# Kernel tuning notes

Measured on AMD Instinct MI355X. Metric: run time of the kernel, lower is better.

Reference implementation:

```python
import jax, jax.numpy as jnp
import numpy as np

SPARSE_COMPRESSION_RATIO = 0.5  # config.sparse_compression_ratio


def setup_inputs() -> dict:
    key = jax.random.key(0)
    kv_cache = jax.random.normal(key, (2, 32, 4096, 128), dtype=jnp.float32)
    return {"kv_cache": kv_cache}


def reference(kv_cache):
    # elements_to_keep = int(numel * (1 - ratio))
    total = kv_cache.size
    k = int(total * (1.0 - SPARSE_COMPRESSION_RATIO))
    flat = kv_cache.reshape(-1)
    # torch.topk(|x|, k, largest=True) -> indices of k largest magnitudes
    _, top_idx = jax.lax.top_k(jnp.abs(flat), k)
    # scatter mask, then elementwise multiply (zeros out non-top-k entries)
    mask = jnp.zeros((total,), dtype=jnp.bool_).at[top_idx].set(True)
    return kv_cache * mask.reshape(kv_cache.shape)
```

## Files before the change

kernel.cpp:

```cpp
#include <hip/hip_runtime.h>
#include <stdint.h>


#define NTHR 256
#define MASK31 0x7fffffffu

#define SH_OFF    0
#define SH_BINS   8192
#define CH_OFF    8192
#define CH_BINS   4096
#define SCL_OFF   12288
#define L3_OFF    12320
#define L3_CAP    4096
#define PAIRS_OFF (L3_OFF + 2 * L3_CAP)
#define PAIRS_CAP 4194304
#define ZERO_WORDS (SCL_OFF + 32)

#define GC_CAP    4096
#define TIE_CAP   1024

__global__ void zero_ws_kernel(uint32_t* __restrict__ ws) {
    int i = blockIdx.x * blockDim.x + threadIdx.x;
    if (i < ZERO_WORDS) ws[i] = 0;
}

__global__ void sample_hist_kernel(const uint4* __restrict__ xv, long long n4,
                                   uint32_t* __restrict__ ws) {
    __shared__ uint32_t lh[SH_BINS];
    for (int i = threadIdx.x; i < SH_BINS; i += NTHR) lh[i] = 0;
    __syncthreads();
    long long S4 = n4 >> 5;
    long long T = (long long)gridDim.x * NTHR;
    for (long long s = (long long)blockIdx.x * NTHR + threadIdx.x; s < S4; s += T) {
        uint4 v = xv[s << 5];
        atomicAdd(&lh[(v.x & MASK31) >> 18], 1u);
        atomicAdd(&lh[(v.y & MASK31) >> 18], 1u);
        atomicAdd(&lh[(v.z & MASK31) >> 18], 1u);
        atomicAdd(&lh[(v.w & MASK31) >> 18], 1u);
    }
    __syncthreads();
    for (int i = threadIdx.x; i < SH_BINS; i += NTHR)
        if (lh[i]) atomicAdd(&ws[SH_OFF + i], lh[i]);
}

__global__ void sel_bracket_kernel(uint32_t* __restrict__ ws,
                                   uint32_t ksmM, uint32_t kspM) {
    __shared__ uint32_t lh[SH_BINS];
    __shared__ uint32_t csum[NTHR];
    __shared__ uint32_t cpre[NTHR];
    __shared__ int sBHi, sB1;
    for (int i = threadIdx.x; i < SH_BINS; i += NTHR) lh[i] = ws[SH_OFF + i];
    if (threadIdx.x == 0) { sBHi = -1; sB1 = -1; }
    __syncthreads();
    uint32_t s = 0;
    for (int i = 0; i < 32; ++i) s += lh[threadIdx.x * 32 + i];
    csum[threadIdx.x] = s;
    __syncthreads();
    if (threadIdx.x == 0) {
        uint32_t run = 0;
        for (int c = NTHR - 1; c >= 0; --c) { cpre[c] = run; run += csum[c]; }
    }
    __syncthreads();
    {
        int c = threadIdx.x;
        int hitHi = -1, hitB1 = -1;
        uint32_t excl = cpre[c];
        for (int bb = c * 32 + 31; bb >= c * 32; --bb) {
            uint32_t cnt = lh[bb];
            uint32_t incl = excl + cnt;
            if (hitHi < 0 && incl >= ksmM) hitHi = bb;
            if (hitB1 < 0 && excl >= kspM) hitB1 = bb;
            excl = incl;
        }
        if (hitHi >= 0) atomicMax(&sBHi, hitHi);
        if (hitB1 >= 0) atomicMax(&sB1, hitB1);
    }
    __syncthreads();
    if (threadIdx.x == 0) {
        int bHi = sBHi < 0 ? 0 : sBHi;
        int bLo = sB1 + 1;
        if (bLo > bHi) bLo = bHi;
        if (bLo < 0) bLo = 0;
        int span = bHi - bLo + 1;
        int clog = 0; while ((1 << clog) < span) ++clog;
        int spanBits = 18 + clog;
        int shift1 = spanBits > 12 ? spanBits - 12 : 0;
        ws[SCL_OFF + 0] = (uint32_t)bLo;
        ws[SCL_OFF + 1] = (uint32_t)bHi;
        ws[SCL_OFF + 2] = (uint32_t)shift1;
        ws[SCL_OFF + 3] = ((uint32_t)bLo) << 18;
    }
}

__global__ void fused_main_kernel(const uint32_t* __restrict__ x,
                                  uint32_t* __restrict__ out, long long n,
                                  uint32_t* __restrict__ ws) {
    __shared__ uint2 stage[GC_CAP];
    __shared__ uint32_t cnt, sHi, base;
    uint32_t bLo = ws[SCL_OFF + 0], bHi = ws[SCL_OFF + 1];
    if (threadIdx.x == 0) { cnt = 0; sHi = 0; }
    __syncthreads();
    uint32_t myHi = 0;
    long long n4 = n >> 2;
    const uint4* xv = (const uint4*)x;
    uint4* ov = (uint4*)out;
    long long stride = (long long)gridDim.x * NTHR;
    for (long long i = (long long)blockIdx.x * NTHR + threadIdx.x; i < n4; i += stride) {
        uint4 v = xv[i];
        uint32_t base4 = (uint32_t)(i << 2);
        uint4 o;
        uint32_t u, b;
        u = v.x & MASK31; b = u >> 18;
        if (b > bHi) { o.x = v.x; ++myHi; }
        else { o.x = 0u; if (b >= bLo) { uint32_t p = atomicAdd(&cnt, 1u); if (p < GC_CAP) stage[p] = make_uint2(v.x, base4 + 0); } }
        u = v.y & MASK31; b = u >> 18;
        if (b > bHi) { o.y = v.y; ++myHi; }
        else { o.y = 0u; if (b >= bLo) { uint32_t p = atomicAdd(&cnt, 1u); if (p < GC_CAP) stage[p] = make_uint2(v.y, base4 + 1); } }
        u = v.z & MASK31; b = u >> 18;
        if (b > bHi) { o.z = v.z; ++myHi; }
        else { o.z = 0u; if (b >= bLo) { uint32_t p = atomicAdd(&cnt, 1u); if (p < GC_CAP) stage[p] = make_uint2(v.z, base4 + 2); } }
        u = v.w & MASK31; b = u >> 18;
        if (b > bHi) { o.w = v.w; ++myHi; }
        else { o.w = 0u; if (b >= bLo) { uint32_t p = atomicAdd(&cnt, 1u); if (p < GC_CAP) stage[p] = make_uint2(v.w, base4 + 3); } }
        ov[i] = o;
    }
    if (blockIdx.x == 0 && threadIdx.x < (int)(n & 3)) {
        long long idx = (n4 << 2) + threadIdx.x;
        uint32_t v = x[idx];
        uint32_t u = v & MASK31, b = u >> 18;
        uint32_t o = 0u;
        if (b > bHi) { o = v; ++myHi; }
        else if (b >= bLo) { uint32_t p = atomicAdd(&cnt, 1u); if (p < GC_CAP) stage[p] = make_uint2(v, (uint32_t)idx); }
        out[idx] = o;
    }
    if (myHi) atomicAdd(&sHi, myHi);
    __syncthreads();
    if (threadIdx.x == 0) {
        uint32_t c = cnt < GC_CAP ? cnt : GC_CAP;
        cnt = c;
        base = atomicAdd(&ws[SCL_OFF + 5], c);
        if (sHi) atomicAdd(&ws[SCL_OFF + 4], sHi);
    }
    __syncthreads();
    uint2* pairs = (uint2*)(ws + PAIRS_OFF);
    uint32_t c = cnt, b0 = base;
    for (uint32_t q = threadIdx.x; q < c; q += NTHR)
        if (b0 + q < PAIRS_CAP) pairs[b0 + q] = stage[q];
}

__global__ void cand_hist_kernel(uint32_t* __restrict__ ws) {
    __shared__ uint32_t lh[CH_BINS];
    uint32_t G = ws[SCL_OFF + 5]; if (G > PAIRS_CAP) G = PAIRS_CAP;
    uint32_t spanBase = ws[SCL_OFF + 3], shift1 = ws[SCL_OFF + 2];
    for (int i = threadIdx.x; i < CH_BINS; i += NTHR) lh[i] = 0;
    __syncthreads();
    const uint2* pairs = (const uint2*)(ws + PAIRS_OFF);
    uint32_t stride = gridDim.x * NTHR;
    for (uint32_t i = blockIdx.x * NTHR + threadIdx.x; i < G; i += stride) {
        uint32_t u = pairs[i].x & MASK31;
        atomicAdd(&lh[((u - spanBase) >> shift1) & (CH_BINS - 1)], 1u);
    }
    __syncthreads();
    for (int i = threadIdx.x; i < CH_BINS; i += NTHR)
        if (lh[i]) atomicAdd(&ws[CH_OFF + i], lh[i]);
}

__global__ void sel_gather_kernel(uint32_t* __restrict__ ws, uint32_t k) {
    __shared__ uint32_t lh[CH_BINS];
    __shared__ uint32_t csum[NTHR];
    __shared__ uint32_t cpre[NTHR];
    __shared__ uint32_t sBase2, sRem2;
    for (int i = threadIdx.x; i < CH_BINS; i += NTHR) lh[i] = ws[CH_OFF + i];
    __syncthreads();
    uint32_t kp = k - ws[SCL_OFF + 4];
    uint32_t s = 0;
    for (int i = 0; i < 16; ++i) s += lh[threadIdx.x * 16 + i];
    csum[threadIdx.x] = s;
    __syncthreads();
    if (threadIdx.x == 0) {
        uint32_t run = 0;
        for (int c = NTHR - 1; c >= 0; --c) { cpre[c] = run; run += csum[c]; }
    }
    __syncthreads();
    if (cpre[threadIdx.x] < kp && kp <= cpre[threadIdx.x] + csum[threadIdx.x]) {
        uint32_t excl = cpre[threadIdx.x];
        for (int bb = threadIdx.x * 16 + 15; bb >= threadIdx.x * 16; --bb) {
            uint32_t cnt = lh[bb];
            if (excl + cnt >= kp) {
                sBase2 = ws[SCL_OFF + 3] + (((uint32_t)bb) << ws[SCL_OFF + 2]);
                sRem2 = kp - excl;
                break;
            }
            excl += cnt;
        }
    }
    __syncthreads();
    if (threadIdx.x == 0) { ws[SCL_OFF + 6] = sBase2; ws[SCL_OFF + 7] = sRem2; }
    uint32_t base2 = sBase2;
    uint32_t width = 1u << ws[SCL_OFF + 2];
    uint32_t G = ws[SCL_OFF + 5]; if (G > PAIRS_CAP) G = PAIRS_CAP;
    const uint2* pairs = (const uint2*)(ws + PAIRS_OFF);
    uint2* l3 = (uint2*)(ws + L3_OFF);
    uint32_t stride = gridDim.x * NTHR;
    for (uint32_t i = blockIdx.x * NTHR + threadIdx.x; i < G; i += stride) {
        uint2 pr = pairs[i];
        uint32_t u = pr.x & MASK31;
        if (u - base2 < width) {
            uint32_t p = atomicAdd(&ws[SCL_OFF + 8], 1u);
            if (p < L3_CAP) l3[p] = pr;
        }
    }
}

__global__ void final_fixup_kernel(uint32_t* __restrict__ ws,
                                   uint32_t* __restrict__ out) {
    __shared__ uint32_t lh[CH_BINS];
    __shared__ uint32_t csum[NTHR];
    __shared__ uint32_t cpre[NTHR];
    __shared__ uint32_t tieIdx[TIE_CAP];
    __shared__ uint32_t tieCnt, sT, sJ, sTieMax;
    uint32_t c3 = ws[SCL_OFF + 8]; if (c3 > L3_CAP) c3 = L3_CAP;
    uint32_t base2 = ws[SCL_OFF + 6], rem2 = ws[SCL_OFF + 7];
    for (int i = threadIdx.x; i < CH_BINS; i += NTHR) lh[i] = 0;
    if (threadIdx.x == 0) tieCnt = 0;
    __syncthreads();
    const uint2* l3 = (const uint2*)(ws + L3_OFF);
    for (uint32_t i = threadIdx.x; i < c3; i += NTHR) {
        uint32_t u = l3[i].x & MASK31;
        atomicAdd(&lh[(u - base2) & (CH_BINS - 1)], 1u);
    }
    __syncthreads();
    uint32_t s = 0;
    for (int i = 0; i < 16; ++i) s += lh[threadIdx.x * 16 + i];
    csum[threadIdx.x] = s;
    __syncthreads();
    if (threadIdx.x == 0) {
        uint32_t run = 0;
        for (int c = NTHR - 1; c >= 0; --c) { cpre[c] = run; run += csum[c]; }
    }
    __syncthreads();
    if (cpre[threadIdx.x] < rem2 && rem2 <= cpre[threadIdx.x] + csum[threadIdx.x]) {
        uint32_t excl = cpre[threadIdx.x];
        for (int bb = threadIdx.x * 16 + 15; bb >= threadIdx.x * 16; --bb) {
            uint32_t cnt = lh[bb];
            if (excl + cnt >= rem2) { sT = base2 + (uint32_t)bb; sJ = rem2 - excl; break; }
            excl += cnt;
        }
    }
    __syncthreads();
    uint32_t t = sT;
    for (uint32_t i = threadIdx.x; i < c3; i += NTHR) {
        uint2 pr = l3[i];
        if ((pr.x & MASK31) == t) {
            uint32_t p = atomicAdd(&tieCnt, 1u);
            if (p < TIE_CAP) tieIdx[p] = pr.y;
        }
    }
    __syncthreads();
    if (threadIdx.x == 0) {
        uint32_t m = tieCnt < TIE_CAP ? tieCnt : TIE_CAP;
        for (uint32_t a = 1; a < m; ++a) {
            uint32_t v = tieIdx[a]; int bp = (int)a - 1;
            while (bp >= 0 && tieIdx[bp] > v) { tieIdx[bp + 1] = tieIdx[bp]; --bp; }
            tieIdx[bp + 1] = v;
        }
        uint32_t j = sJ;
        if (j > m) j = m;
        sJ = j;
        sTieMax = (j > 0) ? tieIdx[j - 1] : 0u;
    }
    __syncthreads();
    uint32_t j = sJ, tieMax = sTieMax;
    uint32_t G = ws[SCL_OFF + 5]; if (G > PAIRS_CAP) G = PAIRS_CAP;
    const uint2* pairs = (const uint2*)(ws + PAIRS_OFF);
    uint32_t stride = gridDim.x * NTHR;
    for (uint32_t i = blockIdx.x * NTHR + threadIdx.x; i < G; i += stride) {
        uint2 pr = pairs[i];
        uint32_t u = pr.x & MASK31;
        bool keep = (u > t) || (u == t && j > 0 && pr.y <= tieMax);
        if (keep) out[pr.y] = pr.x;
    }
}

extern "C" void kernel_launch(void* const* d_in, const int* in_sizes, int n_in,
                              void* d_out, int out_size, void* d_ws, size_t ws_size,
                              hipStream_t stream) {
    const uint32_t* x = (const uint32_t*)d_in[0];
    uint32_t* out = (uint32_t*)d_out;
    uint32_t* ws = (uint32_t*)d_ws;
    long long n = (long long)in_sizes[0];

    const double ratio = 0.5;
    long long k = (long long)((double)n * (1.0 - ratio));
    if (k < 1) k = 1;
    if (k > n) k = n;

    long long n4 = n >> 2;
    long long S = (n4 >> 5) << 2;
    long long ks = (long long)((double)k * ((double)S / (double)n));
    const long long M = 4500;
    uint32_t ksmM = (uint32_t)((ks - M) < 1 ? 1 : (ks - M));
    uint32_t kspM = (uint32_t)((ks + M) > S ? S : (ks + M));

    zero_ws_kernel<<<(ZERO_WORDS + NTHR - 1) / NTHR, NTHR, 0, stream>>>(ws);
    sample_hist_kernel<<<512, NTHR, 0, stream>>>((const uint4*)x, n4, ws);
    sel_bracket_kernel<<<1, NTHR, 0, stream>>>(ws, ksmM, kspM);
    fused_main_kernel<<<2048, NTHR, 0, stream>>>(x, out, n, ws);
    cand_hist_kernel<<<256, NTHR, 0, stream>>>(ws);
    sel_gather_kernel<<<256, NTHR, 0, stream>>>(ws, (uint32_t)k);
    final_fixup_kernel<<<256, NTHR, 0, stream>>>(ws, out);
}
```

Measured before the change: 154.7 us.

## Restructure main pass into one-chunk-per-block with global overflow for candidates

The main filter kernel now gives each block exactly one chunk of four uint4 loads per thread, issued together, in place of a grid-stride loop over 2048 blocks. The shared staging buffer shrinks from 4096 to 512 pairs, and overflow spills straight to the global pair list through an atomic, so more blocks fit per CU. The sample histogram now staggers its sampled offsets within each 32-vector stride, and several small kernels get smaller grids. The aim is more memory-level parallelism and occupancy, at the cost of possible global atomic contention when a block has many candidates.

```diff
diff --git a/kernel.cpp b/kernel.cpp
--- a/kernel.cpp
+++ b/kernel.cpp
@@ -16,7 +16,7 @@
 #define PAIRS_CAP 4194304
 #define ZERO_WORDS (SCL_OFF + 32)
 
-#define GC_CAP    4096
+#define GC_CAP    512
 #define TIE_CAP   1024
 
 __global__ void zero_ws_kernel(uint32_t* __restrict__ ws) {
@@ -32,7 +32,8 @@
     long long S4 = n4 >> 5;
     long long T = (long long)gridDim.x * NTHR;
     for (long long s = (long long)blockIdx.x * NTHR + threadIdx.x; s < S4; s += T) {
-        uint4 v = xv[s << 5];
+        long long idx4 = (s << 5) | (s & 31);
+        uint4 v = xv[idx4];
         atomicAdd(&lh[(v.x & MASK31) >> 18], 1u);
         atomicAdd(&lh[(v.y & MASK31) >> 18], 1u);
         atomicAdd(&lh[(v.z & MASK31) >> 18], 1u);
@@ -92,60 +93,80 @@
     }
 }
 
-__global__ void fused_main_kernel(const uint32_t* __restrict__ x,
-                                  uint32_t* __restrict__ out, long long n,
-                                  uint32_t* __restrict__ ws) {
+__global__ __launch_bounds__(NTHR, 6)
+void fused_main_kernel(const uint32_t* __restrict__ x, uint32_t* __restrict__ out,
+                       long long n, uint32_t* __restrict__ ws) {
     __shared__ uint2 stage[GC_CAP];
-    __shared__ uint32_t cnt, sHi, base;
-    uint32_t bLo = ws[SCL_OFF + 0], bHi = ws[SCL_OFF + 1];
-    if (threadIdx.x == 0) { cnt = 0; sHi = 0; }
+    __shared__ uint32_t cnt, sHi, sBase;
+    const uint32_t bLo = ws[SCL_OFF + 0], bHi = ws[SCL_OFF + 1];
+    const uint32_t bSpan = bHi - bLo;
+    if (threadIdx.x == 0) { cnt = 0u; sHi = 0u; }
     __syncthreads();
     uint32_t myHi = 0;
+    uint2* __restrict__ gpairs = (uint2*)(ws + PAIRS_OFF);
+
+    const uint4* __restrict__ xv = (const uint4*)x;
+    uint4* __restrict__ ov = (uint4*)out;
     long long n4 = n >> 2;
-    const uint4* xv = (const uint4*)x;
-    uint4* ov = (uint4*)out;
-    long long stride = (long long)gridDim.x * NTHR;
-    for (long long i = (long long)blockIdx.x * NTHR + threadIdx.x; i < n4; i += stride) {
-        uint4 v = xv[i];
-        uint32_t base4 = (uint32_t)(i << 2);
-        uint4 o;
-        uint32_t u, b;
-        u = v.x & MASK31; b = u >> 18;
-        if (b > bHi) { o.x = v.x; ++myHi; }
-        else { o.x = 0u; if (b >= bLo) { uint32_t p = atomicAdd(&cnt, 1u); if (p < GC_CAP) stage[p] = make_uint2(v.x, base4 + 0); } }
-        u = v.y & MASK31; b = u >> 18;
-        if (b > bHi) { o.y = v.y; ++myHi; }
-        else { o.y = 0u; if (b >= bLo) { uint32_t p = atomicAdd(&cnt, 1u); if (p < GC_CAP) stage[p] = make_uint2(v.y, base4 + 1); } }
-        u = v.z & MASK31; b = u >> 18;
-        if (b > bHi) { o.z = v.z; ++myHi; }
-        else { o.z = 0u; if (b >= bLo) { uint32_t p = atomicAdd(&cnt, 1u); if (p < GC_CAP) stage[p] = make_uint2(v.z, base4 + 2); } }
-        u = v.w & MASK31; b = u >> 18;
-        if (b > bHi) { o.w = v.w; ++myHi; }
-        else { o.w = 0u; if (b >= bLo) { uint32_t p = atomicAdd(&cnt, 1u); if (p < GC_CAP) stage[p] = make_uint2(v.w, base4 + 3); } }
-        ov[i] = o;
-    }
-    if (blockIdx.x == 0 && threadIdx.x < (int)(n & 3)) {
-        long long idx = (n4 << 2) + threadIdx.x;
-        uint32_t v = x[idx];
-        uint32_t u = v & MASK31, b = u >> 18;
-        uint32_t o = 0u;
-        if (b > bHi) { o = v; ++myHi; }
-        else if (b >= bLo) { uint32_t p = atomicAdd(&cnt, 1u); if (p < GC_CAP) stage[p] = make_uint2(v, (uint32_t)idx); }
-        out[idx] = o;
-    }
+    long long nChunks = n4 / (NTHR * 4);
+
+#define PUSH_PAIR(val, eidx) { \
+    uint32_t p_ = atomicAdd(&cnt, 1u); \
+    uint2 pr_ = make_uint2((val), (eidx)); \
+    if (p_ < GC_CAP) stage[p_] = pr_; \
+    else { uint32_t g_ = atomicAdd(&ws[SCL_OFF + 5], 1u); if (g_ < PAIRS_CAP) gpairs[g_] = pr_; } }
+
+#define COMP(val, eidx) { \
+    uint32_t u_ = (val) & MASK31; uint32_t b_ = u_ >> 18; \
+    uint32_t hi_ = (b_ > bHi) ? 1u : 0u; myHi += hi_; \
+    if (b_ - bLo <= bSpan) PUSH_PAIR((val), (eidx)); \
+    (val) = hi_ ? (val) : 0u; }
+
+    if ((long long)blockIdx.x < nChunks) {
+        long long i0 = (long long)blockIdx.x * (NTHR * 4) + threadIdx.x;
+        uint4 v0 = xv[i0];
+        uint4 v1 = xv[i0 + NTHR];
+        uint4 v2 = xv[i0 + 2 * NTHR];
+        uint4 v3 = xv[i0 + 3 * NTHR];
+        uint32_t e0 = (uint32_t)(i0 << 2);
+        uint32_t e1 = e0 + NTHR * 4;
+        uint32_t e2 = e0 + 2 * NTHR * 4;
+        uint32_t e3 = e0 + 3 * NTHR * 4;
+        COMP(v0.x, e0 + 0) COMP(v0.y, e0 + 1) COMP(v0.z, e0 + 2) COMP(v0.w, e0 + 3)
+        COMP(v1.x, e1 + 0) COMP(v1.y, e1 + 1) COMP(v1.z, e1 + 2) COMP(v1.w, e1 + 3)
+        COMP(v2.x, e2 + 0) COMP(v2.y, e2 + 1) COMP(v2.z, e2 + 2) COMP(v2.w, e2 + 3)
+        COMP(v3.x, e3 + 0) COMP(v3.y, e3 + 1) COMP(v3.z, e3 + 2) COMP(v3.w, e3 + 3)
+        ov[i0]            = v0;
+        ov[i0 + NTHR]     = v1;
+        ov[i0 + 2 * NTHR] = v2;
+        ov[i0 + 3 * NTHR] = v3;
+    }
+
+    long long tailStart = nChunks * (NTHR * 4) * 4;
+    if (blockIdx.x == 0) {
+        for (long long idx = tailStart + threadIdx.x; idx < n; idx += NTHR) {
+            uint32_t v = x[idx];
+            uint32_t u_ = v & MASK31, b_ = u_ >> 18;
+            uint32_t hi_ = (b_ > bHi) ? 1u : 0u; myHi += hi_;
+            if (b_ - bLo <= bSpan) PUSH_PAIR(v, (uint32_t)idx);
+            out[idx] = hi_ ? v : 0u;
+        }
+    }
+
     if (myHi) atomicAdd(&sHi, myHi);
     __syncthreads();
     if (threadIdx.x == 0) {
         uint32_t c = cnt < GC_CAP ? cnt : GC_CAP;
         cnt = c;
-        base = atomicAdd(&ws[SCL_OFF + 5], c);
+        sBase = atomicAdd(&ws[SCL_OFF + 5], c);
         if (sHi) atomicAdd(&ws[SCL_OFF + 4], sHi);
     }
     __syncthreads();
-    uint2* pairs = (uint2*)(ws + PAIRS_OFF);
-    uint32_t c = cnt, b0 = base;
+    uint32_t c = cnt, b0 = sBase;
     for (uint32_t q = threadIdx.x; q < c; q += NTHR)
-        if (b0 + q < PAIRS_CAP) pairs[b0 + q] = stage[q];
+        if (b0 + q < PAIRS_CAP) gpairs[b0 + q] = stage[q];
+#undef COMP
+#undef PUSH_PAIR
 }
 
 __global__ void cand_hist_kernel(uint32_t* __restrict__ ws) {
@@ -302,11 +323,14 @@
     uint32_t ksmM = (uint32_t)((ks - M) < 1 ? 1 : (ks - M));
     uint32_t kspM = (uint32_t)((ks + M) > S ? S : (ks + M));
 
+    long long nChunks = n4 / (NTHR * 4);
+    int grid = (int)(nChunks < 1 ? 1 : nChunks);
+
     zero_ws_kernel<<<(ZERO_WORDS + NTHR - 1) / NTHR, NTHR, 0, stream>>>(ws);
-    sample_hist_kernel<<<512, NTHR, 0, stream>>>((const uint4*)x, n4, ws);
+    sample_hist_kernel<<<128, NTHR, 0, stream>>>((const uint4*)x, n4, ws);
     sel_bracket_kernel<<<1, NTHR, 0, stream>>>(ws, ksmM, kspM);
-    fused_main_kernel<<<2048, NTHR, 0, stream>>>(x, out, n, ws);
-    cand_hist_kernel<<<256, NTHR, 0, stream>>>(ws);
-    sel_gather_kernel<<<256, NTHR, 0, stream>>>(ws, (uint32_t)k);
-    final_fixup_kernel<<<256, NTHR, 0, stream>>>(ws, out);
-}
+    fused_main_kernel<<<grid, NTHR, 0, stream>>>(x, out, n, ws);
+    cand_hist_kernel<<<128, NTHR, 0, stream>>>(ws);
+    sel_gather_kernel<<<128, NTHR, 0, stream>>>(ws, (uint32_t)k);
+    final_fixup_kernel<<<128, NTHR, 0, stream>>>(ws, out);
+}
```

New measurement: 264.6 us. +71.1%, slower.

## Replace candidate compaction with two-pass histogram refine and rank-based tie fixup

Applied to the files above, without the earlier changes.

The single pass that wrote the output and staged every bracket candidate into a global pairs buffer is replaced by two streaming passes over the input. The first pass builds a 1024-bin histogram of the bracketed magnitude range and counts elements above it. A one-block select kernel then picks a narrow threshold bin, and the second pass writes the output while collecting only that bin's few elements. A single-block kernel resolves the boundary bin with an O(m²) rank by value and index. The sample histogram also switches to a strided, spread-out sampling layout. This removes the large candidate shuffling and the multi-kernel gather at the cost of reading the input twice.

```diff
diff --git a/kernel.cpp b/kernel.cpp
--- a/kernel.cpp
+++ b/kernel.cpp
@@ -7,17 +7,12 @@
 
 #define SH_OFF    0
 #define SH_BINS   8192
-#define CH_OFF    8192
-#define CH_BINS   4096
-#define SCL_OFF   12288
-#define L3_OFF    12320
-#define L3_CAP    4096
-#define PAIRS_OFF (L3_OFF + 2 * L3_CAP)
-#define PAIRS_CAP 4194304
-#define ZERO_WORDS (SCL_OFF + 32)
-
-#define GC_CAP    4096
-#define TIE_CAP   1024
+#define BH_OFF    8192
+#define BH_BINS   1024
+#define SCL_OFF   9216
+#define PAIRS_OFF 9232
+#define PAIRS_CAP 8192
+#define ZERO_WORDS (SCL_OFF + 16)
 
 __global__ void zero_ws_kernel(uint32_t* __restrict__ ws) {
     int i = blockIdx.x * blockDim.x + threadIdx.x;
@@ -32,7 +27,9 @@
     long long S4 = n4 >> 5;
     long long T = (long long)gridDim.x * NTHR;
     for (long long s = (long long)blockIdx.x * NTHR + threadIdx.x; s < S4; s += T) {
-        uint4 v = xv[s << 5];
+        long long g = s >> 6;
+        long long idx4 = g * 2048 + ((g & 31) << 6) + (s & 63);
+        uint4 v = xv[idx4];
         atomicAdd(&lh[(v.x & MASK31) >> 18], 1u);
         atomicAdd(&lh[(v.y & MASK31) >> 18], 1u);
         atomicAdd(&lh[(v.z & MASK31) >> 18], 1u);
@@ -81,204 +78,146 @@
         int bLo = sB1 + 1;
         if (bLo > bHi) bLo = bHi;
         if (bLo < 0) bLo = 0;
-        int span = bHi - bLo + 1;
-        int clog = 0; while ((1 << clog) < span) ++clog;
+        int sbins = bHi - bLo + 1;
+        int clog = 0; while ((1 << clog) < sbins) ++clog;
         int spanBits = 18 + clog;
-        int shift1 = spanBits > 12 ? spanBits - 12 : 0;
-        ws[SCL_OFF + 0] = (uint32_t)bLo;
-        ws[SCL_OFF + 1] = (uint32_t)bHi;
+        int shift1 = spanBits - 10;
+        if (shift1 < 0) shift1 = 0;
+        ws[SCL_OFF + 0] = ((uint32_t)bLo) << 18;
+        ws[SCL_OFF + 1] = ((uint32_t)(bHi + 1)) << 18;
         ws[SCL_OFF + 2] = (uint32_t)shift1;
-        ws[SCL_OFF + 3] = ((uint32_t)bLo) << 18;
-    }
-}
-
-__global__ void fused_main_kernel(const uint32_t* __restrict__ x,
-                                  uint32_t* __restrict__ out, long long n,
+    }
+}
+
+__global__ void pass1_hist_kernel(const uint32_t* __restrict__ x, long long n,
                                   uint32_t* __restrict__ ws) {
-    __shared__ uint2 stage[GC_CAP];
-    __shared__ uint32_t cnt, sHi, base;
-    uint32_t bLo = ws[SCL_OFF + 0], bHi = ws[SCL_OFF + 1];
-    if (threadIdx.x == 0) { cnt = 0; sHi = 0; }
-    __syncthreads();
+    __shared__ uint32_t lh[BH_BINS];
+    for (int i = threadIdx.x; i < BH_BINS; i += NTHR) lh[i] = 0;
+    __syncthreads();
+    const uint32_t uLo = ws[SCL_OFF + 0];
+    const uint32_t uHi = ws[SCL_OFF + 1];
+    const uint32_t shift1 = ws[SCL_OFF + 2];
+    const uint32_t span = uHi - uLo;
     uint32_t myHi = 0;
+
+#define DOH(comp) { uint32_t u_ = (comp) & MASK31; \
+    myHi += (u_ >= uHi) ? 1u : 0u; \
+    uint32_t d_ = u_ - uLo; \
+    if (d_ < span) atomicAdd(&lh[(d_ >> shift1) & (BH_BINS - 1)], 1u); }
+
     long long n4 = n >> 2;
-    const uint4* xv = (const uint4*)x;
-    uint4* ov = (uint4*)out;
+    const uint4* __restrict__ xv = (const uint4*)x;
     long long stride = (long long)gridDim.x * NTHR;
     for (long long i = (long long)blockIdx.x * NTHR + threadIdx.x; i < n4; i += stride) {
         uint4 v = xv[i];
-        uint32_t base4 = (uint32_t)(i << 2);
-        uint4 o;
-        uint32_t u, b;
-        u = v.x & MASK31; b = u >> 18;
-        if (b > bHi) { o.x = v.x; ++myHi; }
-        else { o.x = 0u; if (b >= bLo) { uint32_t p = atomicAdd(&cnt, 1u); if (p < GC_CAP) stage[p] = make_uint2(v.x, base4 + 0); } }
-        u = v.y & MASK31; b = u >> 18;
-        if (b > bHi) { o.y = v.y; ++myHi; }
-        else { o.y = 0u; if (b >= bLo) { uint32_t p = atomicAdd(&cnt, 1u); if (p < GC_CAP) stage[p] = make_uint2(v.y, base4 + 1); } }
-        u = v.z & MASK31; b = u >> 18;
-        if (b > bHi) { o.z = v.z; ++myHi; }
-        else { o.z = 0u; if (b >= bLo) { uint32_t p = atomicAdd(&cnt, 1u); if (p < GC_CAP) stage[p] = make_uint2(v.z, base4 + 2); } }
-        u = v.w & MASK31; b = u >> 18;
-        if (b > bHi) { o.w = v.w; ++myHi; }
-        else { o.w = 0u; if (b >= bLo) { uint32_t p = atomicAdd(&cnt, 1u); if (p < GC_CAP) stage[p] = make_uint2(v.w, base4 + 3); } }
-        ov[i] = o;
-    }
-    if (blockIdx.x == 0 && threadIdx.x < (int)(n & 3)) {
-        long long idx = (n4 << 2) + threadIdx.x;
-        uint32_t v = x[idx];
-        uint32_t u = v & MASK31, b = u >> 18;
-        uint32_t o = 0u;
-        if (b > bHi) { o = v; ++myHi; }
-        else if (b >= bLo) { uint32_t p = atomicAdd(&cnt, 1u); if (p < GC_CAP) stage[p] = make_uint2(v, (uint32_t)idx); }
-        out[idx] = o;
-    }
-    if (myHi) atomicAdd(&sHi, myHi);
-    __syncthreads();
-    if (threadIdx.x == 0) {
-        uint32_t c = cnt < GC_CAP ? cnt : GC_CAP;
-        cnt = c;
-        base = atomicAdd(&ws[SCL_OFF + 5], c);
-        if (sHi) atomicAdd(&ws[SCL_OFF + 4], sHi);
-    }
-    __syncthreads();
-    uint2* pairs = (uint2*)(ws + PAIRS_OFF);
-    uint32_t c = cnt, b0 = base;
-    for (uint32_t q = threadIdx.x; q < c; q += NTHR)
-        if (b0 + q < PAIRS_CAP) pairs[b0 + q] = stage[q];
-}
-
-__global__ void cand_hist_kernel(uint32_t* __restrict__ ws) {
-    __shared__ uint32_t lh[CH_BINS];
-    uint32_t G = ws[SCL_OFF + 5]; if (G > PAIRS_CAP) G = PAIRS_CAP;
-    uint32_t spanBase = ws[SCL_OFF + 3], shift1 = ws[SCL_OFF + 2];
-    for (int i = threadIdx.x; i < CH_BINS; i += NTHR) lh[i] = 0;
-    __syncthreads();
-    const uint2* pairs = (const uint2*)(ws + PAIRS_OFF);
-    uint32_t stride = gridDim.x * NTHR;
-    for (uint32_t i = blockIdx.x * NTHR + threadIdx.x; i < G; i += stride) {
-        uint32_t u = pairs[i].x & MASK31;
-        atomicAdd(&lh[((u - spanBase) >> shift1) & (CH_BINS - 1)], 1u);
-    }
-    __syncthreads();
-    for (int i = threadIdx.x; i < CH_BINS; i += NTHR)
-        if (lh[i]) atomicAdd(&ws[CH_OFF + i], lh[i]);
-}
-
-__global__ void sel_gather_kernel(uint32_t* __restrict__ ws, uint32_t k) {
-    __shared__ uint32_t lh[CH_BINS];
+        DOH(v.x) DOH(v.y) DOH(v.z) DOH(v.w)
+    }
+    if (blockIdx.x == 0) {
+        for (long long idx = (n4 << 2) + threadIdx.x; idx < n; idx += NTHR) {
+            uint32_t v = x[idx];
+            DOH(v)
+        }
+    }
+#undef DOH
+    for (int o = 32; o > 0; o >>= 1) myHi += __shfl_down(myHi, o);
+    if ((threadIdx.x & 63) == 0 && myHi) atomicAdd(&ws[SCL_OFF + 3], myHi);
+    __syncthreads();
+    for (int i = threadIdx.x; i < BH_BINS; i += NTHR)
+        if (lh[i]) atomicAdd(&ws[BH_OFF + i], lh[i]);
+}
+
+__global__ void sel2_kernel(uint32_t* __restrict__ ws, uint32_t k) {
+    __shared__ uint32_t lh[BH_BINS];
     __shared__ uint32_t csum[NTHR];
     __shared__ uint32_t cpre[NTHR];
-    __shared__ uint32_t sBase2, sRem2;
-    for (int i = threadIdx.x; i < CH_BINS; i += NTHR) lh[i] = ws[CH_OFF + i];
-    __syncthreads();
-    uint32_t kp = k - ws[SCL_OFF + 4];
+    __shared__ uint32_t sKp;
+    for (int i = threadIdx.x; i < BH_BINS; i += NTHR) lh[i] = ws[BH_OFF + i];
+    __syncthreads();
+    const int cs = BH_BINS / NTHR;
     uint32_t s = 0;
-    for (int i = 0; i < 16; ++i) s += lh[threadIdx.x * 16 + i];
+    for (int i = 0; i < cs; ++i) s += lh[threadIdx.x * cs + i];
     csum[threadIdx.x] = s;
     __syncthreads();
     if (threadIdx.x == 0) {
         uint32_t run = 0;
         for (int c = NTHR - 1; c >= 0; --c) { cpre[c] = run; run += csum[c]; }
-    }
-    __syncthreads();
+        uint32_t cntHi = ws[SCL_OFF + 3];
+        uint32_t total = cpre[0] + csum[0];
+        uint32_t kp = (k > cntHi) ? (k - cntHi) : 1u;
+        if (kp > total) kp = total;
+        if (kp < 1u) kp = 1u;
+        sKp = kp;
+    }
+    __syncthreads();
+    uint32_t kp = sKp;
     if (cpre[threadIdx.x] < kp && kp <= cpre[threadIdx.x] + csum[threadIdx.x]) {
         uint32_t excl = cpre[threadIdx.x];
-        for (int bb = threadIdx.x * 16 + 15; bb >= threadIdx.x * 16; --bb) {
+        for (int bb = threadIdx.x * cs + cs - 1; bb >= threadIdx.x * cs; --bb) {
             uint32_t cnt = lh[bb];
             if (excl + cnt >= kp) {
-                sBase2 = ws[SCL_OFF + 3] + (((uint32_t)bb) << ws[SCL_OFF + 2]);
-                sRem2 = kp - excl;
+                uint32_t uLo = ws[SCL_OFF + 0], shift1 = ws[SCL_OFF + 2];
+                uint32_t tLo = uLo + (((uint32_t)bb) << shift1);
+                ws[SCL_OFF + 5] = tLo;
+                ws[SCL_OFF + 6] = tLo + (1u << shift1);
+                ws[SCL_OFF + 7] = kp - excl;
                 break;
             }
             excl += cnt;
         }
     }
-    __syncthreads();
-    if (threadIdx.x == 0) { ws[SCL_OFF + 6] = sBase2; ws[SCL_OFF + 7] = sRem2; }
-    uint32_t base2 = sBase2;
-    uint32_t width = 1u << ws[SCL_OFF + 2];
-    uint32_t G = ws[SCL_OFF + 5]; if (G > PAIRS_CAP) G = PAIRS_CAP;
-    const uint2* pairs = (const uint2*)(ws + PAIRS_OFF);
-    uint2* l3 = (uint2*)(ws + L3_OFF);
-    uint32_t stride = gridDim.x * NTHR;
-    for (uint32_t i = blockIdx.x * NTHR + threadIdx.x; i < G; i += stride) {
-        uint2 pr = pairs[i];
-        uint32_t u = pr.x & MASK31;
-        if (u - base2 < width) {
-            uint32_t p = atomicAdd(&ws[SCL_OFF + 8], 1u);
-            if (p < L3_CAP) l3[p] = pr;
-        }
-    }
+}
+
+__global__ void pass2_out_kernel(const uint32_t* __restrict__ x,
+                                 uint32_t* __restrict__ out, long long n,
+                                 uint32_t* __restrict__ ws) {
+    const uint32_t tLo = ws[SCL_OFF + 5];
+    const uint32_t tHi2 = ws[SCL_OFF + 6];
+    const uint32_t W = tHi2 - tLo;
+    uint2* __restrict__ gpairs = (uint2*)(ws + PAIRS_OFF);
+
+#define DOC(comp, eidx) { uint32_t u_ = (comp) & MASK31; \
+    if (u_ - tLo < W) { uint32_t p_ = atomicAdd(&ws[SCL_OFF + 4], 1u); \
+        if (p_ < PAIRS_CAP) gpairs[p_] = make_uint2((comp), (eidx)); } \
+    (comp) = (u_ >= tHi2) ? (comp) : 0u; }
+
+    long long n4 = n >> 2;
+    const uint4* __restrict__ xv = (const uint4*)x;
+    uint4* __restrict__ ov = (uint4*)out;
+    long long stride = (long long)gridDim.x * NTHR;
+    for (long long i = (long long)blockIdx.x * NTHR + threadIdx.x; i < n4; i += stride) {
+        uint4 v = xv[i];
+        uint32_t e0 = (uint32_t)(i << 2);
+        DOC(v.x, e0 + 0u) DOC(v.y, e0 + 1u) DOC(v.z, e0 + 2u) DOC(v.w, e0 + 3u)
+        ov[i] = v;
+    }
+    if (blockIdx.x == 0) {
+        for (long long idx = (n4 << 2) + threadIdx.x; idx < n; idx += NTHR) {
+            uint32_t v = x[idx];
+            DOC(v, (uint32_t)idx)
+            out[idx] = v;
+        }
+    }
+#undef DOC
 }
 
 __global__ void final_fixup_kernel(uint32_t* __restrict__ ws,
                                    uint32_t* __restrict__ out) {
-    __shared__ uint32_t lh[CH_BINS];
-    __shared__ uint32_t csum[NTHR];
-    __shared__ uint32_t cpre[NTHR];
-    __shared__ uint32_t tieIdx[TIE_CAP];
-    __shared__ uint32_t tieCnt, sT, sJ, sTieMax;
-    uint32_t c3 = ws[SCL_OFF + 8]; if (c3 > L3_CAP) c3 = L3_CAP;
-    uint32_t base2 = ws[SCL_OFF + 6], rem2 = ws[SCL_OFF + 7];
-    for (int i = threadIdx.x; i < CH_BINS; i += NTHR) lh[i] = 0;
-    if (threadIdx.x == 0) tieCnt = 0;
-    __syncthreads();
-    const uint2* l3 = (const uint2*)(ws + L3_OFF);
-    for (uint32_t i = threadIdx.x; i < c3; i += NTHR) {
-        uint32_t u = l3[i].x & MASK31;
-        atomicAdd(&lh[(u - base2) & (CH_BINS - 1)], 1u);
-    }
-    __syncthreads();
-    uint32_t s = 0;
-    for (int i = 0; i < 16; ++i) s += lh[threadIdx.x * 16 + i];
-    csum[threadIdx.x] = s;
-    __syncthreads();
-    if (threadIdx.x == 0) {
-        uint32_t run = 0;
-        for (int c = NTHR - 1; c >= 0; --c) { cpre[c] = run; run += csum[c]; }
-    }
-    __syncthreads();
-    if (cpre[threadIdx.x] < rem2 && rem2 <= cpre[threadIdx.x] + csum[threadIdx.x]) {
-        uint32_t excl = cpre[threadIdx.x];
-        for (int bb = threadIdx.x * 16 + 15; bb >= threadIdx.x * 16; --bb) {
-            uint32_t cnt = lh[bb];
-            if (excl + cnt >= rem2) { sT = base2 + (uint32_t)bb; sJ = rem2 - excl; break; }
-            excl += cnt;
-        }
-    }
-    __syncthreads();
-    uint32_t t = sT;
-    for (uint32_t i = threadIdx.x; i < c3; i += NTHR) {
-        uint2 pr = l3[i];
-        if ((pr.x & MASK31) == t) {
-            uint32_t p = atomicAdd(&tieCnt, 1u);
-            if (p < TIE_CAP) tieIdx[p] = pr.y;
-        }
-    }
-    __syncthreads();
-    if (threadIdx.x == 0) {
-        uint32_t m = tieCnt < TIE_CAP ? tieCnt : TIE_CAP;
-        for (uint32_t a = 1; a < m; ++a) {
-            uint32_t v = tieIdx[a]; int bp = (int)a - 1;
-            while (bp >= 0 && tieIdx[bp] > v) { tieIdx[bp + 1] = tieIdx[bp]; --bp; }
-            tieIdx[bp + 1] = v;
-        }
-        uint32_t j = sJ;
-        if (j > m) j = m;
-        sJ = j;
-        sTieMax = (j > 0) ? tieIdx[j - 1] : 0u;
-    }
-    __syncthreads();
-    uint32_t j = sJ, tieMax = sTieMax;
-    uint32_t G = ws[SCL_OFF + 5]; if (G > PAIRS_CAP) G = PAIRS_CAP;
-    const uint2* pairs = (const uint2*)(ws + PAIRS_OFF);
-    uint32_t stride = gridDim.x * NTHR;
-    for (uint32_t i = blockIdx.x * NTHR + threadIdx.x; i < G; i += stride) {
-        uint2 pr = pairs[i];
-        uint32_t u = pr.x & MASK31;
-        bool keep = (u > t) || (u == t && j > 0 && pr.y <= tieMax);
-        if (keep) out[pr.y] = pr.x;
+    __shared__ uint2 lp[PAIRS_CAP];
+    uint32_t m = ws[SCL_OFF + 4]; if (m > PAIRS_CAP) m = PAIRS_CAP;
+    uint32_t remB = ws[SCL_OFF + 7];
+    const uint2* __restrict__ gpairs = (const uint2*)(ws + PAIRS_OFF);
+    for (uint32_t i = threadIdx.x; i < m; i += NTHR) lp[i] = gpairs[i];
+    __syncthreads();
+    for (uint32_t i = threadIdx.x; i < m; i += NTHR) {
+        uint2 me = lp[i];
+        uint32_t ui = me.x & MASK31;
+        uint32_t rank = 0;
+        for (uint32_t p = 0; p < m; ++p) {
+            uint2 pr = lp[p];
+            uint32_t up = pr.x & MASK31;
+            rank += (up > ui || (up == ui && pr.y < me.y)) ? 1u : 0u;
+        }
+        if (rank < remB) out[me.y] = me.x;
     }
 }
 
@@ -303,10 +242,10 @@
     uint32_t kspM = (uint32_t)((ks + M) > S ? S : (ks + M));
 
     zero_ws_kernel<<<(ZERO_WORDS + NTHR - 1) / NTHR, NTHR, 0, stream>>>(ws);
-    sample_hist_kernel<<<512, NTHR, 0, stream>>>((const uint4*)x, n4, ws);
+    sample_hist_kernel<<<256, NTHR, 0, stream>>>((const uint4*)x, n4, ws);
     sel_bracket_kernel<<<1, NTHR, 0, stream>>>(ws, ksmM, kspM);
-    fused_main_kernel<<<2048, NTHR, 0, stream>>>(x, out, n, ws);
-    cand_hist_kernel<<<256, NTHR, 0, stream>>>(ws);
-    sel_gather_kernel<<<256, NTHR, 0, stream>>>(ws, (uint32_t)k);
-    final_fixup_kernel<<<256, NTHR, 0, stream>>>(ws, out);
-}
+    pass1_hist_kernel<<<2048, NTHR, 0, stream>>>(x, n, ws);
+    sel2_kernel<<<1, NTHR, 0, stream>>>(ws, (uint32_t)k);
+    pass2_out_kernel<<<2048, NTHR, 0, stream>>>(x, out, n, ws);
+    final_fixup_kernel<<<1, NTHR, 0, stream>>>(ws, out);
+}
```

Measured after the change: 237.6 us. 1.54x slower.
